# Kernel optimization log

Measured on AMD Instinct MI355X. Metric: run time of the kernel, lower is better.

## Reference

```python
import jax, jax.numpy as jnp
import numpy as np

B, N, D, H = 2, 2048, 1024, 16
DH = D // H
SCALE = DH ** -0.5

def setup_inputs() -> dict:
    key = jax.random.key(0)
    k1, k2, k3 = jax.random.split(key, 3)
    x = jax.random.normal(k1, (B, N, D), dtype=jnp.float32)
    W_qkv = jax.random.normal(k2, (3 * D, D), dtype=jnp.float32) * (D ** -0.5)
    W_out = jax.random.normal(k3, (D, D), dtype=jnp.float32) * (D ** -0.5)
    mask = jnp.tril(jnp.ones((N, N), dtype=jnp.int32))  # causal mask; 0 -> -inf
    return {"x": x, "mask": mask, "W_qkv": W_qkv, "W_out": W_out}

def reference(x, mask, W_qkv, W_out):
    b, n, d = x.shape
    qkv = x @ W_qkv.T                                   # [B,N,3D]
    qkv = qkv.reshape(b, n, 3, H, DH).transpose(2, 0, 3, 1, 4)  # [3,B,H,N,DH]
    q, k, v = qkv[0], qkv[1], qkv[2]
    attn = jnp.einsum('bhqd,bhkd->bhqk', q, k) * SCALE  # [B,H,N,N]
    attn = jnp.where(mask == 0, -jnp.inf, attn)
    attn = jax.nn.softmax(attn, axis=-1)
    out = jnp.einsum('bhqk,bhkd->bhqd', attn, v)        # [B,H,N,DH]
    out = out.transpose(0, 2, 1, 3).reshape(b, n, d)    # [B,N,D]
    return out @ W_out.T
```

## Files before the change

kernel.cpp:

```cpp
#include <hip/hip_runtime.h>
#include <hip/hip_bf16.h>


typedef __hip_bfloat16 bf16;
typedef short bf16x8 __attribute__((ext_vector_type(8)));
typedef short bf16x4 __attribute__((ext_vector_type(4)));
typedef float f32x4 __attribute__((ext_vector_type(4)));

#define QSCALE 0.1803368801111204f

typedef __attribute__((address_space(3))) unsigned int lds_u32;
typedef const __attribute__((address_space(1))) unsigned int glob_u32;

__device__ __forceinline__ void glds16(const void* g, void* l) {
    __builtin_amdgcn_global_load_lds((glob_u32*)g, (lds_u32*)l, 16, 0, 0);
}

__device__ __forceinline__ short f2bf(float f) {
    __hip_bfloat16 h = __float2bfloat16(f);
    return *reinterpret_cast<short*>(&h);
}

__device__ __forceinline__ unsigned pack_bf16(float a, float b) {
    unsigned au = __builtin_bit_cast(unsigned, a) + 0x8000u;
    unsigned bu = __builtin_bit_cast(unsigned, b) + 0x8000u;
    return __builtin_amdgcn_perm(bu, au, 0x07060302u);
}

__global__ void cast_all(const float* __restrict__ x, const float* __restrict__ wqkv,
                         const float* __restrict__ wout,
                         bf16* __restrict__ xb, bf16* __restrict__ wqkvb,
                         bf16* __restrict__ woutb) {
    int i = blockIdx.x * blockDim.x + threadIdx.x;
    const float4* s; short4* d; int o;
    if (i < 1048576)               { s = (const float4*)x;    d = (short4*)xb;    o = i; }
    else if (i < 1835008)          { s = (const float4*)wqkv; d = (short4*)wqkvb; o = i - 1048576; }
    else                           { s = (const float4*)wout; d = (short4*)woutb; o = i - 1835008; }
    float4 f = s[o];
    short4 v;
    v.x = f2bf(f.x); v.y = f2bf(f.y); v.z = f2bf(f.z); v.w = f2bf(f.w);
    d[o] = v;
}

template<int EPI>
__global__ __launch_bounds__(256)
void gemm128(const bf16* __restrict__ A, const bf16* __restrict__ Bt,
             float* __restrict__ Cf,
             bf16* __restrict__ qp, bf16* __restrict__ kp, bf16* __restrict__ vp,
             int K, int Ncols) {
    __shared__ alignas(16) short As[2][4096];
    __shared__ alignas(16) short Bs[2][4096];

    const int tid = threadIdx.x;
    const int wave = tid >> 6, lane = tid & 63;
    const int quad = lane >> 4, l16 = lane & 15;
    const int wm = wave >> 1, wn = wave & 1;
    const int m0 = blockIdx.x * 128;
    const int n0 = blockIdx.y * 128;

    f32x4 acc[4][4] = {};

    const int srow = tid >> 2;
    const int skk  = (((tid & 3) ^ ((tid >> 3) & 3))) * 8;
    const bf16* Ag = A  + (size_t)(m0 + srow) * K + skk;
    const bf16* Bg = Bt + (size_t)(n0 + srow) * K + skk;
    const size_t rowskip = (size_t)64 * K;
    short* Asl = &As[0][0] + tid * 8;
    short* Bsl = &Bs[0][0] + tid * 8;

    const int xk = (quad ^ ((l16 >> 1) & 3)) * 8;
    const int arow = wm * 64 + l16;
    const int brow = wn * 64 + l16;

    const int KI = K >> 5;
    glds16(Ag, Asl);
    glds16(Ag + rowskip, Asl + 2048);
    glds16(Bg, Bsl);
    glds16(Bg + rowskip, Bsl + 2048);
    __syncthreads();

    int buf = 0;
    for (int ki = 0; ki < KI; ++ki) {
        if (ki + 1 < KI) {
            const bf16* ag = Ag + (ki + 1) * 32;
            const bf16* bg = Bg + (ki + 1) * 32;
            short* ad = Asl + (buf ^ 1) * 4096;
            short* bd = Bsl + (buf ^ 1) * 4096;
            glds16(ag, ad);
            glds16(ag + rowskip, ad + 2048);
            glds16(bg, bd);
            glds16(bg + rowskip, bd + 2048);
        }
        const short* ab = &As[buf][0];
        const short* bb = &Bs[buf][0];
        bf16x8 af[4], bf[4];
        #pragma unroll
        for (int mt = 0; mt < 4; ++mt)
            af[mt] = *reinterpret_cast<const bf16x8*>(ab + (arow + mt * 16) * 32 + xk);
        #pragma unroll
        for (int nt = 0; nt < 4; ++nt)
            bf[nt] = *reinterpret_cast<const bf16x8*>(bb + (brow + nt * 16) * 32 + xk);
        #pragma unroll
        for (int mt = 0; mt < 4; ++mt)
            #pragma unroll
            for (int nt = 0; nt < 4; ++nt)
                acc[mt][nt] = __builtin_amdgcn_mfma_f32_16x16x32_bf16(
                    af[mt], bf[nt], acc[mt][nt], 0, 0, 0);
        __syncthreads();
        buf ^= 1;
    }

    #pragma unroll
    for (int mt = 0; mt < 4; ++mt) {
        #pragma unroll
        for (int nt = 0; nt < 4; ++nt) {
            #pragma unroll
            for (int r = 0; r < 4; ++r) {
                int gm = m0 + wm * 64 + mt * 16 + quad * 4 + r;
                int gn = n0 + wn * 64 + nt * 16 + l16;
                float val = acc[mt][nt][r];
                if (EPI == 0) {
                    int sel = gn >> 10, rem = gn & 1023;
                    int h = rem >> 6, dh = rem & 63;
                    int b = gm >> 11, nq = gm & 2047;
                    if (sel == 0) val *= QSCALE;
                    bf16* dst = (sel == 0) ? qp : ((sel == 1) ? kp : vp);
                    dst[((((size_t)b * 16 + h) * 2048) + nq) * 64 + dh] = __float2bfloat16(val);
                } else {
                    Cf[(size_t)gm * Ncols + gn] = val;
                }
            }
        }
    }
}

__global__ __launch_bounds__(256, 2)
void flash_attn(const bf16* __restrict__ Q, const bf16* __restrict__ K,
                const bf16* __restrict__ V, bf16* __restrict__ O) {
    __shared__ alignas(16) short Ks[2][128][72];
    __shared__ alignas(16) short Vt[2][64][132];

    const int tid = threadIdx.x;
    const int wave = tid >> 6, lane = tid & 63;
    const int quad = lane >> 4, l16 = lane & 15;
    const int bh = blockIdx.x;
    const int yy = blockIdx.y;
    const int qt = (yy < 8) ? yy : (15 - (yy & 7));
    const int Q0 = qt * 128;
    const float NEG_INF = -__builtin_inff();

    const bf16* Qb = Q + (size_t)bh * 2048 * 64;
    const bf16* Kb = K + (size_t)bh * 2048 * 64;
    const bf16* Vb = V + (size_t)bh * 2048 * 64;

    const int qrowA = Q0 + wave * 16 + l16;
    const int qrowB = qrowA + 64;
    const bf16x8 qfA0 = *reinterpret_cast<const bf16x8*>(Qb + (size_t)qrowA * 64 + quad * 8);
    const bf16x8 qfA1 = *reinterpret_cast<const bf16x8*>(Qb + (size_t)qrowA * 64 + 32 + quad * 8);
    const bf16x8 qfB0 = *reinterpret_cast<const bf16x8*>(Qb + (size_t)qrowB * 64 + quad * 8);
    const bf16x8 qfB1 = *reinterpret_cast<const bf16x8*>(Qb + (size_t)qrowB * 64 + 32 + quad * 8);

    float lA = 0.f, lB = 0.f;
    f32x4 oA[4] = {}, oB[4] = {};

    const int krow = tid >> 2;
    const int kcol = (tid & 3) * 16;
    const int kb   = (tid & 15) * 4;
    const int db   = (tid >> 4) * 4;

    {
        #pragma unroll
        for (int g = 0; g < 2; ++g) {
            const bf16* kr = Kb + (size_t)(g * 64 + krow) * 64 + kcol;
            *reinterpret_cast<bf16x8*>(&Ks[0][g * 64 + krow][kcol])     = *reinterpret_cast<const bf16x8*>(kr);
            *reinterpret_cast<bf16x8*>(&Ks[0][g * 64 + krow][kcol + 8]) = *reinterpret_cast<const bf16x8*>(kr + 8);
        }
        #pragma unroll
        for (int g = 0; g < 2; ++g) {
            const int kbg = g * 64 + kb;
            bf16x4 L0 = *reinterpret_cast<const bf16x4*>(Vb + (size_t)(kbg + 0) * 64 + db);
            bf16x4 L1 = *reinterpret_cast<const bf16x4*>(Vb + (size_t)(kbg + 1) * 64 + db);
            bf16x4 L2 = *reinterpret_cast<const bf16x4*>(Vb + (size_t)(kbg + 2) * 64 + db);
            bf16x4 L3 = *reinterpret_cast<const bf16x4*>(Vb + (size_t)(kbg + 3) * 64 + db);
            #pragma unroll
            for (int j = 0; j < 4; ++j) {
                bf16x4 w; w[0] = L0[j]; w[1] = L1[j]; w[2] = L2[j]; w[3] = L3[j];
                *reinterpret_cast<bf16x4*>(&Vt[0][db + j][kbg]) = w;
            }
        }
    }
    __syncthreads();

    int buf = 0;
    for (int j0 = 0; j0 < Q0; j0 += 128) {
        const bf16* Kn = Kb + (size_t)(j0 + 128) * 64;
        const bf16* Vn = Vb + (size_t)(j0 + 128) * 64;
        bf16x8 nk[2][2];
        bf16x4 NV[2][4];
        #pragma unroll
        for (int g = 0; g < 2; ++g) {
            const bf16* kr = Kn + (size_t)(g * 64 + krow) * 64 + kcol;
            nk[g][0] = *reinterpret_cast<const bf16x8*>(kr);
            nk[g][1] = *reinterpret_cast<const bf16x8*>(kr + 8);
            const int kbg = g * 64 + kb;
            #pragma unroll
            for (int j = 0; j < 4; ++j)
                NV[g][j] = *reinterpret_cast<const bf16x4*>(Vn + (size_t)(kbg + j) * 64 + db);
        }

        bf16x4 pkA[8], pkB[8];
        f32x4 sA, sB, sAn, sBn;
        {
            bf16x8 k0 = *reinterpret_cast<const bf16x8*>(&Ks[buf][l16][quad * 8]);
            bf16x8 k1 = *reinterpret_cast<const bf16x8*>(&Ks[buf][l16][32 + quad * 8]);
            __builtin_amdgcn_s_setprio(1);
            sA = {}; sB = {};
            sA = __builtin_amdgcn_mfma_f32_16x16x32_bf16(k0, qfA0, sA, 0, 0, 0);
            sA = __builtin_amdgcn_mfma_f32_16x16x32_bf16(k1, qfA1, sA, 0, 0, 0);
            sB = __builtin_amdgcn_mfma_f32_16x16x32_bf16(k0, qfB0, sB, 0, 0, 0);
            sB = __builtin_amdgcn_mfma_f32_16x16x32_bf16(k1, qfB1, sB, 0, 0, 0);
            __builtin_amdgcn_s_setprio(0);
        }
        #pragma unroll
        for (int t = 0; t < 8; ++t) {
            if (t < 7) {
                bf16x8 k0 = *reinterpret_cast<const bf16x8*>(&Ks[buf][16 * (t + 1) + l16][quad * 8]);
                bf16x8 k1 = *reinterpret_cast<const bf16x8*>(&Ks[buf][16 * (t + 1) + l16][32 + quad * 8]);
                __builtin_amdgcn_s_setprio(1);
                sAn = {}; sBn = {};
                sAn = __builtin_amdgcn_mfma_f32_16x16x32_bf16(k0, qfA0, sAn, 0, 0, 0);
                sAn = __builtin_amdgcn_mfma_f32_16x16x32_bf16(k1, qfA1, sAn, 0, 0, 0);
                sBn = __builtin_amdgcn_mfma_f32_16x16x32_bf16(k0, qfB0, sBn, 0, 0, 0);
                sBn = __builtin_amdgcn_mfma_f32_16x16x32_bf16(k1, qfB1, sBn, 0, 0, 0);
                __builtin_amdgcn_s_setprio(0);
            }
            float a0 = __builtin_amdgcn_exp2f(sA[0]);
            float a1 = __builtin_amdgcn_exp2f(sA[1]);
            float a2 = __builtin_amdgcn_exp2f(sA[2]);
            float a3 = __builtin_amdgcn_exp2f(sA[3]);
            float b0 = __builtin_amdgcn_exp2f(sB[0]);
            float b1 = __builtin_amdgcn_exp2f(sB[1]);
            float b2 = __builtin_amdgcn_exp2f(sB[2]);
            float b3 = __builtin_amdgcn_exp2f(sB[3]);
            lA += (a0 + a1) + (a2 + a3);
            lB += (b0 + b1) + (b2 + b3);
            unsigned* pa = reinterpret_cast<unsigned*>(&pkA[t]);
            pa[0] = pack_bf16(a0, a1); pa[1] = pack_bf16(a2, a3);
            unsigned* pb = reinterpret_cast<unsigned*>(&pkB[t]);
            pb[0] = pack_bf16(b0, b1); pb[1] = pack_bf16(b2, b3);
            if (t > 0) {
                __builtin_amdgcn_s_setprio(1);
                #pragma unroll
                for (int dt = 0; dt < 4; ++dt) {
                    bf16x4 vf = *reinterpret_cast<const bf16x4*>(
                        &Vt[buf][dt * 16 + l16][(t - 1) * 16 + quad * 4]);
                    oA[dt] = __builtin_amdgcn_mfma_f32_16x16x16bf16_1k(vf, pkA[t - 1], oA[dt], 0, 0, 0);
                    oB[dt] = __builtin_amdgcn_mfma_f32_16x16x16bf16_1k(vf, pkB[t - 1], oB[dt], 0, 0, 0);
                }
                __builtin_amdgcn_s_setprio(0);
            }
            if (t < 7) { sA = sAn; sB = sBn; }
        }

        #pragma unroll
        for (int g = 0; g < 2; ++g) {
            *reinterpret_cast<bf16x8*>(&Ks[buf ^ 1][g * 64 + krow][kcol])     = nk[g][0];
            *reinterpret_cast<bf16x8*>(&Ks[buf ^ 1][g * 64 + krow][kcol + 8]) = nk[g][1];
            const int kbg = g * 64 + kb;
            #pragma unroll
            for (int j = 0; j < 4; ++j) {
                bf16x4 w; w[0] = NV[g][0][j]; w[1] = NV[g][1][j]; w[2] = NV[g][2][j]; w[3] = NV[g][3][j];
                *reinterpret_cast<bf16x4*>(&Vt[buf ^ 1][db + j][kbg]) = w;
            }
        }

        {
            __builtin_amdgcn_s_setprio(1);
            #pragma unroll
            for (int dt = 0; dt < 4; ++dt) {
                bf16x4 vf = *reinterpret_cast<const bf16x4*>(
                    &Vt[buf][dt * 16 + l16][7 * 16 + quad * 4]);
                oA[dt] = __builtin_amdgcn_mfma_f32_16x16x16bf16_1k(vf, pkA[7], oA[dt], 0, 0, 0);
                oB[dt] = __builtin_amdgcn_mfma_f32_16x16x16bf16_1k(vf, pkB[7], oB[dt], 0, 0, 0);
            }
            __builtin_amdgcn_s_setprio(0);
        }
        __syncthreads();
        buf ^= 1;
    }

    {
        bf16x4 pkA[8], pkB[8];
        #pragma unroll
        for (int t = 0; t < 8; ++t) {
            const bool actB = (t <= wave + 4);
            const bool actA = (t <= wave);
            if (actB) {
                bf16x8 k0 = *reinterpret_cast<const bf16x8*>(&Ks[buf][16 * t + l16][quad * 8]);
                bf16x8 k1 = *reinterpret_cast<const bf16x8*>(&Ks[buf][16 * t + l16][32 + quad * 8]);
                f32x4 sB = {};
                sB = __builtin_amdgcn_mfma_f32_16x16x32_bf16(k0, qfB0, sB, 0, 0, 0);
                sB = __builtin_amdgcn_mfma_f32_16x16x32_bf16(k1, qfB1, sB, 0, 0, 0);
                if (t == wave + 4) {
                    #pragma unroll
                    for (int r = 0; r < 4; ++r)
                        if (quad * 4 + r > l16) sB[r] = NEG_INF;
                }
                float b0 = __builtin_amdgcn_exp2f(sB[0]);
                float b1 = __builtin_amdgcn_exp2f(sB[1]);
                float b2 = __builtin_amdgcn_exp2f(sB[2]);
                float b3 = __builtin_amdgcn_exp2f(sB[3]);
                lB += (b0 + b1) + (b2 + b3);
                unsigned* pb = reinterpret_cast<unsigned*>(&pkB[t]);
                pb[0] = pack_bf16(b0, b1); pb[1] = pack_bf16(b2, b3);
                if (actA) {
                    f32x4 sA = {};
                    sA = __builtin_amdgcn_mfma_f32_16x16x32_bf16(k0, qfA0, sA, 0, 0, 0);
                    sA = __builtin_amdgcn_mfma_f32_16x16x32_bf16(k1, qfA1, sA, 0, 0, 0);
                    if (t == wave) {
                        #pragma unroll
                        for (int r = 0; r < 4; ++r)
                            if (quad * 4 + r > l16) sA[r] = NEG_INF;
                    }
                    float a0 = __builtin_amdgcn_exp2f(sA[0]);
                    float a1 = __builtin_amdgcn_exp2f(sA[1]);
                    float a2 = __builtin_amdgcn_exp2f(sA[2]);
                    float a3 = __builtin_amdgcn_exp2f(sA[3]);
                    lA += (a0 + a1) + (a2 + a3);
                    unsigned* pa = reinterpret_cast<unsigned*>(&pkA[t]);
                    pa[0] = pack_bf16(a0, a1); pa[1] = pack_bf16(a2, a3);
                }
            }
        }
        #pragma unroll
        for (int t = 0; t < 8; ++t) {
            if (t <= wave + 4) {
                #pragma unroll
                for (int dt = 0; dt < 4; ++dt) {
                    bf16x4 vf = *reinterpret_cast<const bf16x4*>(
                        &Vt[buf][dt * 16 + l16][t * 16 + quad * 4]);
                    oB[dt] = __builtin_amdgcn_mfma_f32_16x16x16bf16_1k(vf, pkB[t], oB[dt], 0, 0, 0);
                    if (t <= wave)
                        oA[dt] = __builtin_amdgcn_mfma_f32_16x16x16bf16_1k(vf, pkA[t], oA[dt], 0, 0, 0);
                }
            }
        }
    }

    lA += __shfl_xor(lA, 16, 64);
    lA += __shfl_xor(lA, 32, 64);
    lB += __shfl_xor(lB, 16, 64);
    lB += __shfl_xor(lB, 32, 64);
    const float invA = 1.f / lA;
    const float invB = 1.f / lB;

    const int b = bh >> 4, h = bh & 15;
    bf16* orowA = O + ((size_t)b * 2048 + qrowA) * 1024 + h * 64;
    bf16* orowB = O + ((size_t)b * 2048 + qrowB) * 1024 + h * 64;
    #pragma unroll
    for (int dt = 0; dt < 4; ++dt) {
        bf16x4 wA, wB;
        unsigned* ua = reinterpret_cast<unsigned*>(&wA);
        ua[0] = pack_bf16(oA[dt][0] * invA, oA[dt][1] * invA);
        ua[1] = pack_bf16(oA[dt][2] * invA, oA[dt][3] * invA);
        *reinterpret_cast<bf16x4*>(orowA + dt * 16 + quad * 4) = wA;
        unsigned* ub = reinterpret_cast<unsigned*>(&wB);
        ub[0] = pack_bf16(oB[dt][0] * invB, oB[dt][1] * invB);
        ub[1] = pack_bf16(oB[dt][2] * invB, oB[dt][3] * invB);
        *reinterpret_cast<bf16x4*>(orowB + dt * 16 + quad * 4) = wB;
    }
}

extern "C" void kernel_launch(void* const* d_in, const int* in_sizes, int n_in,
                              void* d_out, int out_size, void* d_ws, size_t ws_size,
                              hipStream_t stream) {
    const float* x    = (const float*)d_in[0];
    const float* Wqkv = (const float*)d_in[2];
    const float* Wout = (const float*)d_in[3];
    float* out = (float*)d_out;

    char* ws = (char*)d_ws;
    bf16* x_bf    = (bf16*)(ws);
    bf16* wqkv_bf = (bf16*)(ws + 8388608);
    bf16* wout_bf = (bf16*)(ws + 14680064);
    bf16* q       = (bf16*)(ws + 16777216);
    bf16* k       = (bf16*)(ws + 25165824);
    bf16* v       = (bf16*)(ws + 33554432);
    bf16* ao      = (bf16*)(ws + 41943040);

    cast_all<<<8192, 256, 0, stream>>>(x, Wqkv, Wout, x_bf, wqkv_bf, wout_bf);
    gemm128<0><<<dim3(32, 24), 256, 0, stream>>>(x_bf, wqkv_bf, nullptr, q, k, v, 1024, 3072);
    flash_attn<<<dim3(32, 16), 256, 0, stream>>>(q, k, v, ao);
    gemm128<1><<<dim3(32, 8), 256, 0, stream>>>(ao, wout_bf, out, nullptr, nullptr, nullptr, 1024, 1024);
}
```

Baseline: 179.2 us.

## Use 128x64 tiles for output GEMM and preload K fragments in attention

The output projection gets its own kernel with 128x64 tiles, which doubles the grid from 256 to 512 blocks so more CUs have work on the 1024-wide output. In flash attention, all eight K-tile fragments are loaded from LDS into registers up front instead of one per step inside the loop. This is meant to shorten LDS latency stalls between MFMAs. The cost is higher register pressure in a kernel bounded to two blocks per CU, and less reuse per tile in the GEMM.

Measured after the change: 177.8 us, median of 2. About the same (-0.8%).

```diff
diff --git a/kernel.cpp b/kernel.cpp
--- a/kernel.cpp
+++ b/kernel.cpp
@@ -42,12 +42,10 @@
     d[o] = v;
 }
 
-template<int EPI>
 __global__ __launch_bounds__(256)
-void gemm128(const bf16* __restrict__ A, const bf16* __restrict__ Bt,
-             float* __restrict__ Cf,
-             bf16* __restrict__ qp, bf16* __restrict__ kp, bf16* __restrict__ vp,
-             int K, int Ncols) {
+void gemm128_qkv(const bf16* __restrict__ A, const bf16* __restrict__ Bt,
+                 bf16* __restrict__ qp, bf16* __restrict__ kp, bf16* __restrict__ vp,
+                 int K) {
     __shared__ alignas(16) short As[2][4096];
     __shared__ alignas(16) short Bs[2][4096];
 
@@ -119,16 +117,89 @@
                 int gm = m0 + wm * 64 + mt * 16 + quad * 4 + r;
                 int gn = n0 + wn * 64 + nt * 16 + l16;
                 float val = acc[mt][nt][r];
-                if (EPI == 0) {
-                    int sel = gn >> 10, rem = gn & 1023;
-                    int h = rem >> 6, dh = rem & 63;
-                    int b = gm >> 11, nq = gm & 2047;
-                    if (sel == 0) val *= QSCALE;
-                    bf16* dst = (sel == 0) ? qp : ((sel == 1) ? kp : vp);
-                    dst[((((size_t)b * 16 + h) * 2048) + nq) * 64 + dh] = __float2bfloat16(val);
-                } else {
-                    Cf[(size_t)gm * Ncols + gn] = val;
-                }
+                int sel = gn >> 10, rem = gn & 1023;
+                int h = rem >> 6, dh = rem & 63;
+                int b = gm >> 11, nq = gm & 2047;
+                if (sel == 0) val *= QSCALE;
+                bf16* dst = (sel == 0) ? qp : ((sel == 1) ? kp : vp);
+                dst[((((size_t)b * 16 + h) * 2048) + nq) * 64 + dh] = __float2bfloat16(val);
+            }
+        }
+    }
+}
+
+__global__ __launch_bounds__(256)
+void gemm_out(const bf16* __restrict__ A, const bf16* __restrict__ Bt,
+              float* __restrict__ Cf, int K, int Ncols) {
+    __shared__ alignas(16) short As[2][4096];
+    __shared__ alignas(16) short Bs[2][2048];
+
+    const int tid = threadIdx.x;
+    const int wave = tid >> 6, lane = tid & 63;
+    const int quad = lane >> 4, l16 = lane & 15;
+    const int wm = wave >> 1, wn = wave & 1;
+    const int m0 = blockIdx.x * 128;
+    const int n0 = blockIdx.y * 64;
+
+    f32x4 acc[4][2] = {};
+
+    const int srow = tid >> 2;
+    const int skk  = (((tid & 3) ^ ((tid >> 3) & 3))) * 8;
+    const bf16* Ag = A  + (size_t)(m0 + srow) * K + skk;
+    const bf16* Bg = Bt + (size_t)(n0 + srow) * K + skk;
+    const size_t rowskip = (size_t)64 * K;
+    short* Asl = &As[0][0] + tid * 8;
+    short* Bsl = &Bs[0][0] + tid * 8;
+
+    const int xk = (quad ^ ((l16 >> 1) & 3)) * 8;
+    const int arow = wm * 64 + l16;
+    const int brow = wn * 32 + l16;
+
+    const int KI = K >> 5;
+    glds16(Ag, Asl);
+    glds16(Ag + rowskip, Asl + 2048);
+    glds16(Bg, Bsl);
+    __syncthreads();
+
+    int buf = 0;
+    for (int ki = 0; ki < KI; ++ki) {
+        if (ki + 1 < KI) {
+            const bf16* ag = Ag + (ki + 1) * 32;
+            const bf16* bg = Bg + (ki + 1) * 32;
+            short* ad = Asl + (buf ^ 1) * 4096;
+            short* bd = Bsl + (buf ^ 1) * 2048;
+            glds16(ag, ad);
+            glds16(ag + rowskip, ad + 2048);
+            glds16(bg, bd);
+        }
+        const short* ab = &As[buf][0];
+        const short* bb = &Bs[buf][0];
+        bf16x8 af[4], bf[2];
+        #pragma unroll
+        for (int mt = 0; mt < 4; ++mt)
+            af[mt] = *reinterpret_cast<const bf16x8*>(ab + (arow + mt * 16) * 32 + xk);
+        #pragma unroll
+        for (int nt = 0; nt < 2; ++nt)
+            bf[nt] = *reinterpret_cast<const bf16x8*>(bb + (brow + nt * 16) * 32 + xk);
+        #pragma unroll
+        for (int mt = 0; mt < 4; ++mt)
+            #pragma unroll
+            for (int nt = 0; nt < 2; ++nt)
+                acc[mt][nt] = __builtin_amdgcn_mfma_f32_16x16x32_bf16(
+                    af[mt], bf[nt], acc[mt][nt], 0, 0, 0);
+        __syncthreads();
+        buf ^= 1;
+    }
+
+    #pragma unroll
+    for (int mt = 0; mt < 4; ++mt) {
+        #pragma unroll
+        for (int nt = 0; nt < 2; ++nt) {
+            #pragma unroll
+            for (int r = 0; r < 4; ++r) {
+                int gm = m0 + wm * 64 + mt * 16 + quad * 4 + r;
+                int gn = n0 + wn * 32 + nt * 16 + l16;
+                Cf[(size_t)gm * Ncols + gn] = acc[mt][nt][r];
             }
         }
     }
@@ -208,30 +279,33 @@
                 NV[g][j] = *reinterpret_cast<const bf16x4*>(Vn + (size_t)(kbg + j) * 64 + db);
         }
 
+        bf16x8 kf[8][2];
+        #pragma unroll
+        for (int t = 0; t < 8; ++t) {
+            kf[t][0] = *reinterpret_cast<const bf16x8*>(&Ks[buf][16 * t + l16][quad * 8]);
+            kf[t][1] = *reinterpret_cast<const bf16x8*>(&Ks[buf][16 * t + l16][32 + quad * 8]);
+        }
+
         bf16x4 pkA[8], pkB[8];
         f32x4 sA, sB, sAn, sBn;
         {
-            bf16x8 k0 = *reinterpret_cast<const bf16x8*>(&Ks[buf][l16][quad * 8]);
-            bf16x8 k1 = *reinterpret_cast<const bf16x8*>(&Ks[buf][l16][32 + quad * 8]);
             __builtin_amdgcn_s_setprio(1);
             sA = {}; sB = {};
-            sA = __builtin_amdgcn_mfma_f32_16x16x32_bf16(k0, qfA0, sA, 0, 0, 0);
-            sA = __builtin_amdgcn_mfma_f32_16x16x32_bf16(k1, qfA1, sA, 0, 0, 0);
-            sB = __builtin_amdgcn_mfma_f32_16x16x32_bf16(k0, qfB0, sB, 0, 0, 0);
-            sB = __builtin_amdgcn_mfma_f32_16x16x32_bf16(k1, qfB1, sB, 0, 0, 0);
+            sA = __builtin_amdgcn_mfma_f32_16x16x32_bf16(kf[0][0], qfA0, sA, 0, 0, 0);
+            sA = __builtin_amdgcn_mfma_f32_16x16x32_bf16(kf[0][1], qfA1, sA, 0, 0, 0);
+            sB = __builtin_amdgcn_mfma_f32_16x16x32_bf16(kf[0][0], qfB0, sB, 0, 0, 0);
+            sB = __builtin_amdgcn_mfma_f32_16x16x32_bf16(kf[0][1], qfB1, sB, 0, 0, 0);
             __builtin_amdgcn_s_setprio(0);
         }
         #pragma unroll
         for (int t = 0; t < 8; ++t) {
             if (t < 7) {
-                bf16x8 k0 = *reinterpret_cast<const bf16x8*>(&Ks[buf][16 * (t + 1) + l16][quad * 8]);
-                bf16x8 k1 = *reinterpret_cast<const bf16x8*>(&Ks[buf][16 * (t + 1) + l16][32 + quad * 8]);
                 __builtin_amdgcn_s_setprio(1);
                 sAn = {}; sBn = {};
-                sAn = __builtin_amdgcn_mfma_f32_16x16x32_bf16(k0, qfA0, sAn, 0, 0, 0);
-                sAn = __builtin_amdgcn_mfma_f32_16x16x32_bf16(k1, qfA1, sAn, 0, 0, 0);
-                sBn = __builtin_amdgcn_mfma_f32_16x16x32_bf16(k0, qfB0, sBn, 0, 0, 0);
-                sBn = __builtin_amdgcn_mfma_f32_16x16x32_bf16(k1, qfB1, sBn, 0, 0, 0);
+                sAn = __builtin_amdgcn_mfma_f32_16x16x32_bf16(kf[t + 1][0], qfA0, sAn, 0, 0, 0);
+                sAn = __builtin_amdgcn_mfma_f32_16x16x32_bf16(kf[t + 1][1], qfA1, sAn, 0, 0, 0);
+                sBn = __builtin_amdgcn_mfma_f32_16x16x32_bf16(kf[t + 1][0], qfB0, sBn, 0, 0, 0);
+                sBn = __builtin_amdgcn_mfma_f32_16x16x32_bf16(kf[t + 1][1], qfB1, sBn, 0, 0, 0);
                 __builtin_amdgcn_s_setprio(0);
             }
             float a0 = __builtin_amdgcn_exp2f(sA[0]);
@@ -389,7 +463,7 @@
     bf16* ao      = (bf16*)(ws + 41943040);
 
     cast_all<<<8192, 256, 0, stream>>>(x, Wqkv, Wout, x_bf, wqkv_bf, wout_bf);
-    gemm128<0><<<dim3(32, 24), 256, 0, stream>>>(x_bf, wqkv_bf, nullptr, q, k, v, 1024, 3072);
+    gemm128_qkv<<<dim3(32, 24), 256, 0, stream>>>(x_bf, wqkv_bf, q, k, v, 1024);
     flash_attn<<<dim3(32, 16), 256, 0, stream>>>(q, k, v, ao);
-    gemm128<1><<<dim3(32, 8), 256, 0, stream>>>(ao, wout_bf, out, nullptr, nullptr, nullptr, 1024, 1024);
-}
+    gemm_out<<<dim3(32, 16), 256, 0, stream>>>(ao, wout_bf, out, 1024, 1024);
+}
```
